# Optimization experiments

Hardware: AMD Instinct MI355X
Metric: run time of the kernel (lower is better)

## Reference

```python
import jax, jax.numpy as jnp
import numpy as np

PATCH = 9
EMBED = 768

def setup_inputs() -> dict:
    key = jax.random.key(0)
    k1, k2, k3, k4, k5, k6 = jax.random.split(key, 6)
    B, T, C, H, W = 4, 16, 3, 256, 256
    N = 8192
    patch_dim = PATCH * PATCH * C  # 243
    frames = jax.random.normal(k1, (B, T, C, H, W), dtype=jnp.float32)
    coords = jax.random.uniform(k2, (B, N, 2), dtype=jnp.float32)
    t_src = jax.random.randint(k3, (B, N), 0, T, dtype=jnp.int32)
    # MLP params (Linear: y = x @ W + b), kaiming-ish scale
    W1 = jax.random.normal(k4, (patch_dim, EMBED), dtype=jnp.float32) / np.sqrt(patch_dim)
    b1 = jnp.zeros((EMBED,), dtype=jnp.float32)
    W2 = jax.random.normal(k5, (EMBED, EMBED), dtype=jnp.float32) / np.sqrt(EMBED)
    b2 = jnp.zeros((EMBED,), dtype=jnp.float32)
    return {"frames": frames, "coords": coords, "t_src": t_src,
            "W1": W1, "b1": b1, "W2": W2, "b2": b2}

def reference(frames, coords, t_src, W1, b1, W2, b2):
    B, T, C, H, W = frames.shape
    N = coords.shape[1]
    half = PATCH // 2
    # integer center pixel (coords in [0,1] -> truncation == floor for nonneg)
    u = (coords[..., 0] * (W - 1)).astype(jnp.int32)  # (B, N)
    v = (coords[..., 1] * (H - 1)).astype(jnp.int32)
    off = jnp.arange(PATCH, dtype=jnp.int32) - half    # (P,)
    # replicate padding at borders == clamped gather indices
    ys = jnp.clip(v[..., None] + off, 0, H - 1)        # (B, N, P)
    xs = jnp.clip(u[..., None] + off, 0, W - 1)        # (B, N, P)
    fp = jnp.transpose(frames, (0, 1, 3, 4, 2))        # (B, T, H, W, C)
    bidx = jnp.arange(B, dtype=jnp.int32)[:, None, None, None]
    # gather patches: (B, N, P, P, C)
    patches = fp[bidx, t_src[:, :, None, None].astype(jnp.int32),
                 ys[:, :, :, None], xs[:, :, None, :]]
    x = patches.reshape(B, N, PATCH * PATCH * C)       # (B, N, 243)
    h = jax.nn.gelu(x @ W1 + b1, approximate=False)    # torch nn.GELU = exact erf
    return h @ W2 + b2                                 # (B, N, EMBED)
```

## Files before the change

### kernel.cpp

```cpp
#include <hip/hip_runtime.h>
#include <math.h>


typedef __attribute__((ext_vector_type(8))) short short8;
typedef __attribute__((ext_vector_type(4))) float floatx4;

#define M_ROWS 32768
#define KPAD   256
#define EMB    768

typedef __attribute__((address_space(1))) const void g_void;
typedef __attribute__((address_space(3))) void l_void;

__device__ __forceinline__ unsigned short f2bf(float f) {
    union { float f; unsigned int i; } w;
    w.f = f;
    unsigned int x = w.i;
    x += 0x7fffu + ((x >> 16) & 1u);
    return (unsigned short)(x >> 16);
}

__device__ __forceinline__ float gelu_f(float x) {
    float x3 = x * x * x;
    float y  = 1.5957691216f * (x + 0.044715f * x3);
    float e  = __expf(y);
    float th = 1.0f - 2.0f / (e + 1.0f);
    return 0.5f * x * (1.0f + th);
}

__global__ void k_transpose_w1(const float* __restrict__ W1,
                               unsigned short* __restrict__ W1T) {
    int idx = blockIdx.x * 256 + threadIdx.x;
    int n  = idx >> 8;
    int kp = idx & 255;
    unsigned short v = 0;
    if (kp < 243) {
        int c = kp / 81;
        int r = kp - c * 81;
        int i = r / 9;
        int j = r - i * 9;
        int e = i * 27 + j * 3 + c;
        v = f2bf(W1[e * EMB + n]);
    }
    W1T[idx] = v;
}

__global__ void k_transpose_w2(const float* __restrict__ W2,
                               unsigned short* __restrict__ W2T) {
    __shared__ float tile[32][33];
    int tx = threadIdx.x & 31, ty = threadIdx.x >> 5;
    int k0 = blockIdx.x * 32, n0 = blockIdx.y * 32;
#pragma unroll
    for (int i = 0; i < 4; ++i)
        tile[ty + i * 8][tx] = W2[(size_t)(k0 + ty + i * 8) * EMB + n0 + tx];
    __syncthreads();
#pragma unroll
    for (int i = 0; i < 4; ++i)
        W2T[(size_t)(n0 + ty + i * 8) * EMB + k0 + tx] = f2bf(tile[tx][ty + i * 8]);
}

__global__ void k_gather(const float* __restrict__ frames,
                         const float* __restrict__ coords,
                         const int* __restrict__ t_src,
                         unsigned short* __restrict__ X) {
    int row  = blockIdx.x * 4 + (threadIdx.x >> 6);
    int lane = threadIdx.x & 63;
    int b = row >> 13;

    float cu = coords[row * 2 + 0];
    float cv = coords[row * 2 + 1];
    int u = (int)(cu * 255.0f);
    int v = (int)(cv * 255.0f);
    int t = t_src[row];

    const float* fb = frames + (size_t)(b * 16 + t) * (3 * 256 * 256);
    unsigned short* xr = X + (size_t)row * KPAD;

#pragma unroll
    for (int it = 0; it < 4; ++it) {
        int kp = lane + it * 64;
        unsigned short val = 0;
        if (kp < 243) {
            int c = kp / 81;
            int r = kp - c * 81;
            int i = r / 9;
            int j = r - i * 9;
            int y = v + i - 4; y = (y < 0) ? 0 : (y > 255 ? 255 : y);
            int x = u + j - 4; x = (x < 0) ? 0 : (x > 255 ? 255 : x);
            val = f2bf(fb[(size_t)c * 65536 + y * 256 + x]);
        }
        xr[kp] = val;
    }
}

template <int K, bool GELU_, bool OUT_F32>
static __device__ __forceinline__
void gemm_body(const unsigned short* __restrict__ A,
               const unsigned short* __restrict__ BT,
               const float* __restrict__ bias,
               void* __restrict__ Cv) {
    __shared__ unsigned short As[2][128 * 64];
    __shared__ unsigned short Bs[2][128 * 64];

    const int tid  = threadIdx.x;
    const int wave = tid >> 6;
    const int lane = tid & 63;
    const int wr = wave >> 2;
    const int wc = wave & 3;
    const int lm = lane & 15;
    const int lq = lane >> 4;

    const int bid = blockIdx.x;
    const int swz = (bid & 7) * 192 + (bid >> 3);
    const int by  = swz % 6;
    const int bx  = swz / 6;
    const int m0 = bx * 128;
    const int n0 = by * 128;

    floatx4 acc[4][2];
#pragma unroll
    for (int i = 0; i < 4; ++i)
#pragma unroll
        for (int j = 0; j < 2; ++j)
            acc[i][j] = (floatx4){0.f, 0.f, 0.f, 0.f};

    const unsigned short* Ag = A  + (size_t)m0 * K;
    const unsigned short* Bg = BT + (size_t)n0 * K;

    const int rl    = lane >> 3;
    const int pl    = lane & 7;
    const int lslot = pl ^ rl;
    const int c0 = wave;
    const int c1 = 8 + wave;
    const size_t o0 = (size_t)(c0 * 8 + rl) * K + (lslot << 3);
    const size_t o1 = (size_t)(c1 * 8 + rl) * K + (lslot << 3);

    __builtin_amdgcn_global_load_lds((g_void*)(Ag + o0), (l_void*)(&As[0][c0 * 512]), 16, 0, 0);
    __builtin_amdgcn_global_load_lds((g_void*)(Ag + o1), (l_void*)(&As[0][c1 * 512]), 16, 0, 0);
    __builtin_amdgcn_global_load_lds((g_void*)(Bg + o0), (l_void*)(&Bs[0][c0 * 512]), 16, 0, 0);
    __builtin_amdgcn_global_load_lds((g_void*)(Bg + o1), (l_void*)(&Bs[0][c1 * 512]), 16, 0, 0);

    int buf = 0;
    for (int k0 = 0; k0 < K; k0 += 64) {
        __syncthreads();

        if (k0 + 64 < K) {
            __builtin_amdgcn_global_load_lds((g_void*)(Ag + o0 + k0 + 64),
                                             (l_void*)(&As[buf ^ 1][c0 * 512]), 16, 0, 0);
            __builtin_amdgcn_global_load_lds((g_void*)(Ag + o1 + k0 + 64),
                                             (l_void*)(&As[buf ^ 1][c1 * 512]), 16, 0, 0);
            __builtin_amdgcn_global_load_lds((g_void*)(Bg + o0 + k0 + 64),
                                             (l_void*)(&Bs[buf ^ 1][c0 * 512]), 16, 0, 0);
            __builtin_amdgcn_global_load_lds((g_void*)(Bg + o1 + k0 + 64),
                                             (l_void*)(&Bs[buf ^ 1][c1 * 512]), 16, 0, 0);
        }

#pragma unroll
        for (int ks = 0; ks < 2; ++ks) {
            short8 af[4], bfr[2];
#pragma unroll
            for (int mi = 0; mi < 4; ++mi) {
                int row = wr * 64 + mi * 16 + lm;
                int ps  = ((ks << 2) + lq) ^ (row & 7);
                af[mi] = *(const short8*)(&As[buf][row * 64 + (ps << 3)]);
            }
#pragma unroll
            for (int ni = 0; ni < 2; ++ni) {
                int row = wc * 32 + ni * 16 + lm;
                int ps  = ((ks << 2) + lq) ^ (row & 7);
                bfr[ni] = *(const short8*)(&Bs[buf][row * 64 + (ps << 3)]);
            }
#pragma unroll
            for (int mi = 0; mi < 4; ++mi)
#pragma unroll
                for (int ni = 0; ni < 2; ++ni)
                    acc[mi][ni] = __builtin_amdgcn_mfma_f32_16x16x32_bf16(
                        af[mi], bfr[ni], acc[mi][ni], 0, 0, 0);
        }
        buf ^= 1;
    }

#pragma unroll
    for (int ni = 0; ni < 2; ++ni) {
        int col = n0 + wc * 32 + ni * 16 + lm;
        float bs = bias[col];
#pragma unroll
        for (int mi = 0; mi < 4; ++mi) {
            int rowb = m0 + wr * 64 + mi * 16 + lq * 4;
#pragma unroll
            for (int r = 0; r < 4; ++r) {
                float x = acc[mi][ni][r] + bs;
                if (GELU_)
                    x = gelu_f(x);
                size_t idx = (size_t)(rowb + r) * EMB + col;
                if (OUT_F32)
                    ((float*)Cv)[idx] = x;
                else
                    ((unsigned short*)Cv)[idx] = f2bf(x);
            }
        }
    }
}

__global__ __launch_bounds__(512, 4)
void k_gemm1(const unsigned short* __restrict__ A, const unsigned short* __restrict__ BT,
             const float* __restrict__ bias, unsigned short* __restrict__ C) {
    gemm_body<KPAD, true, false>(A, BT, bias, (void*)C);
}

__global__ __launch_bounds__(512, 4)
void k_gemm2(const unsigned short* __restrict__ A, const unsigned short* __restrict__ BT,
             const float* __restrict__ bias, float* __restrict__ C) {
    gemm_body<EMB, false, true>(A, BT, bias, (void*)C);
}

extern "C" void kernel_launch(void* const* d_in, const int* in_sizes, int n_in,
                              void* d_out, int out_size, void* d_ws, size_t ws_size,
                              hipStream_t stream) {
    const float* frames = (const float*)d_in[0];
    const float* coords = (const float*)d_in[1];
    const int*   t_src  = (const int*)d_in[2];
    const float* W1     = (const float*)d_in[3];
    const float* b1     = (const float*)d_in[4];
    const float* W2     = (const float*)d_in[5];
    const float* b2     = (const float*)d_in[6];
    float* out = (float*)d_out;

    char* ws = (char*)d_ws;
    unsigned short* X    = (unsigned short*)(ws);
    unsigned short* Hbuf = (unsigned short*)(ws + 16777216);
    unsigned short* W1T  = (unsigned short*)(ws + 16777216 + 50331648);
    unsigned short* W2T  = (unsigned short*)(ws + 16777216 + 50331648 + 393216);

    k_transpose_w1<<<768, 256, 0, stream>>>(W1, W1T);
    k_transpose_w2<<<dim3(24, 24), 256, 0, stream>>>(W2, W2T);

    k_gather<<<M_ROWS / 4, 256, 0, stream>>>(frames, coords, t_src, X);

    k_gemm1<<<1536, 512, 0, stream>>>(X, W1T, b1, Hbuf);

    k_gemm2<<<1536, 512, 0, stream>>>(Hbuf, W2T, b2, out);
}
```

Baseline: 228.7 us.

## Restructure GEMM to 4 waves with 64x64 warp tiles and K-step 32

Reworks the GEMM kernels from 8 waves with 64x32 per-wave tiles and K-step 64 to 4 waves with 64x64 per-wave tiles and K-step 32. LDS gets a new swizzled layout and the fragment offsets are precomputed, which halves LDS use and raises register reuse per fragment load. Output stores switch to nontemporal writes to avoid polluting cache. The trade-off is more loop iterations and barriers per K, plus fewer threads per block to hide latency.

Result: slower. 286.8 us (+25.4%).

```diff
diff --git a/kernel.cpp b/kernel.cpp
--- a/kernel.cpp
+++ b/kernel.cpp
@@ -1,6 +1,8 @@
 #include <hip/hip_runtime.h>
 #include <math.h>
 
+
+#define USE_NT 1
 
 typedef __attribute__((ext_vector_type(8))) short short8;
 typedef __attribute__((ext_vector_type(4))) float floatx4;
@@ -99,14 +101,14 @@
                const unsigned short* __restrict__ BT,
                const float* __restrict__ bias,
                void* __restrict__ Cv) {
-    __shared__ unsigned short As[2][128 * 64];
-    __shared__ unsigned short Bs[2][128 * 64];
+    __shared__ unsigned short As[2][128 * 32];
+    __shared__ unsigned short Bs[2][128 * 32];
 
     const int tid  = threadIdx.x;
     const int wave = tid >> 6;
     const int lane = tid & 63;
-    const int wr = wave >> 2;
-    const int wc = wave & 3;
+    const int wm = (wave >> 1) * 64;
+    const int wn = (wave & 1) * 64;
     const int lm = lane & 15;
     const int lq = lane >> 4;
 
@@ -117,23 +119,30 @@
     const int m0 = bx * 128;
     const int n0 = by * 128;
 
-    floatx4 acc[4][2];
+    floatx4 acc[4][4];
 #pragma unroll
     for (int i = 0; i < 4; ++i)
 #pragma unroll
-        for (int j = 0; j < 2; ++j)
+        for (int j = 0; j < 4; ++j)
             acc[i][j] = (floatx4){0.f, 0.f, 0.f, 0.f};
 
     const unsigned short* Ag = A  + (size_t)m0 * K;
     const unsigned short* Bg = BT + (size_t)n0 * K;
 
-    const int rl    = lane >> 3;
-    const int pl    = lane & 7;
-    const int lslot = pl ^ rl;
-    const int c0 = wave;
-    const int c1 = 8 + wave;
-    const size_t o0 = (size_t)(c0 * 8 + rl) * K + (lslot << 3);
-    const size_t o1 = (size_t)(c1 * 8 + rl) * K + (lslot << 3);
+    const int rloc   = 2 * (lane >> 3) + ((lane >> 2) & 1);
+    const int kchunk = (lane & 3) ^ ((lane >> 3) & 3);
+    const int c0 = 2 * wave, c1 = 2 * wave + 1;
+    const size_t o0 = (size_t)(c0 * 16 + rloc) * K + (kchunk << 3);
+    const size_t o1 = (size_t)(c1 * 16 + rloc) * K + (kchunk << 3);
+
+    int aoff[4], boff[4];
+#pragma unroll
+    for (int mi = 0; mi < 4; ++mi) {
+        int r = wm + mi * 16 + lm;
+        aoff[mi] = (r >> 1) * 64 + (r & 1) * 32 + ((lq ^ ((r >> 1) & 3)) << 3);
+        int rb = wn + mi * 16 + lm;
+        boff[mi] = (rb >> 1) * 64 + (rb & 1) * 32 + ((lq ^ ((rb >> 1) & 3)) << 3);
+    }
 
     __builtin_amdgcn_global_load_lds((g_void*)(Ag + o0), (l_void*)(&As[0][c0 * 512]), 16, 0, 0);
     __builtin_amdgcn_global_load_lds((g_void*)(Ag + o1), (l_void*)(&As[0][c1 * 512]), 16, 0, 0);
@@ -141,74 +150,76 @@
     __builtin_amdgcn_global_load_lds((g_void*)(Bg + o1), (l_void*)(&Bs[0][c1 * 512]), 16, 0, 0);
 
     int buf = 0;
-    for (int k0 = 0; k0 < K; k0 += 64) {
+#pragma unroll 2
+    for (int k0 = 0; k0 < K; k0 += 32) {
         __syncthreads();
 
-        if (k0 + 64 < K) {
-            __builtin_amdgcn_global_load_lds((g_void*)(Ag + o0 + k0 + 64),
+        if (k0 + 32 < K) {
+            __builtin_amdgcn_global_load_lds((g_void*)(Ag + o0 + k0 + 32),
                                              (l_void*)(&As[buf ^ 1][c0 * 512]), 16, 0, 0);
-            __builtin_amdgcn_global_load_lds((g_void*)(Ag + o1 + k0 + 64),
+            __builtin_amdgcn_global_load_lds((g_void*)(Ag + o1 + k0 + 32),
                                              (l_void*)(&As[buf ^ 1][c1 * 512]), 16, 0, 0);
-            __builtin_amdgcn_global_load_lds((g_void*)(Bg + o0 + k0 + 64),
+            __builtin_amdgcn_global_load_lds((g_void*)(Bg + o0 + k0 + 32),
                                              (l_void*)(&Bs[buf ^ 1][c0 * 512]), 16, 0, 0);
-            __builtin_amdgcn_global_load_lds((g_void*)(Bg + o1 + k0 + 64),
+            __builtin_amdgcn_global_load_lds((g_void*)(Bg + o1 + k0 + 32),
                                              (l_void*)(&Bs[buf ^ 1][c1 * 512]), 16, 0, 0);
         }
 
-#pragma unroll
-        for (int ks = 0; ks < 2; ++ks) {
-            short8 af[4], bfr[2];
-#pragma unroll
-            for (int mi = 0; mi < 4; ++mi) {
-                int row = wr * 64 + mi * 16 + lm;
-                int ps  = ((ks << 2) + lq) ^ (row & 7);
-                af[mi] = *(const short8*)(&As[buf][row * 64 + (ps << 3)]);
-            }
-#pragma unroll
-            for (int ni = 0; ni < 2; ++ni) {
-                int row = wc * 32 + ni * 16 + lm;
-                int ps  = ((ks << 2) + lq) ^ (row & 7);
-                bfr[ni] = *(const short8*)(&Bs[buf][row * 64 + (ps << 3)]);
-            }
-#pragma unroll
-            for (int mi = 0; mi < 4; ++mi)
-#pragma unroll
-                for (int ni = 0; ni < 2; ++ni)
-                    acc[mi][ni] = __builtin_amdgcn_mfma_f32_16x16x32_bf16(
-                        af[mi], bfr[ni], acc[mi][ni], 0, 0, 0);
-        }
+        short8 af[4], bfr[4];
+#pragma unroll
+        for (int mi = 0; mi < 4; ++mi)
+            af[mi] = *(const short8*)(&As[buf][aoff[mi]]);
+#pragma unroll
+        for (int ni = 0; ni < 4; ++ni)
+            bfr[ni] = *(const short8*)(&Bs[buf][boff[ni]]);
+
+#pragma unroll
+        for (int mi = 0; mi < 4; ++mi)
+#pragma unroll
+            for (int ni = 0; ni < 4; ++ni)
+                acc[mi][ni] = __builtin_amdgcn_mfma_f32_16x16x32_bf16(
+                    af[mi], bfr[ni], acc[mi][ni], 0, 0, 0);
         buf ^= 1;
     }
 
 #pragma unroll
-    for (int ni = 0; ni < 2; ++ni) {
-        int col = n0 + wc * 32 + ni * 16 + lm;
+    for (int ni = 0; ni < 4; ++ni) {
+        int col = n0 + wn + ni * 16 + lm;
         float bs = bias[col];
 #pragma unroll
         for (int mi = 0; mi < 4; ++mi) {
-            int rowb = m0 + wr * 64 + mi * 16 + lq * 4;
+            int rowb = m0 + wm + mi * 16 + lq * 4;
 #pragma unroll
             for (int r = 0; r < 4; ++r) {
                 float x = acc[mi][ni][r] + bs;
                 if (GELU_)
                     x = gelu_f(x);
                 size_t idx = (size_t)(rowb + r) * EMB + col;
-                if (OUT_F32)
+                if (OUT_F32) {
+#if USE_NT
+                    __builtin_nontemporal_store(x, &((float*)Cv)[idx]);
+#else
                     ((float*)Cv)[idx] = x;
-                else
+#endif
+                } else {
+#if USE_NT
+                    __builtin_nontemporal_store(f2bf(x), &((unsigned short*)Cv)[idx]);
+#else
                     ((unsigned short*)Cv)[idx] = f2bf(x);
+#endif
+                }
             }
         }
     }
 }
 
-__global__ __launch_bounds__(512, 4)
+__global__ __launch_bounds__(256, 4)
 void k_gemm1(const unsigned short* __restrict__ A, const unsigned short* __restrict__ BT,
              const float* __restrict__ bias, unsigned short* __restrict__ C) {
     gemm_body<KPAD, true, false>(A, BT, bias, (void*)C);
 }
 
-__global__ __launch_bounds__(512, 4)
+__global__ __launch_bounds__(256, 4)
 void k_gemm2(const unsigned short* __restrict__ A, const unsigned short* __restrict__ BT,
              const float* __restrict__ bias, float* __restrict__ C) {
     gemm_body<EMB, false, true>(A, BT, bias, (void*)C);
@@ -237,7 +248,7 @@
 
     k_gather<<<M_ROWS / 4, 256, 0, stream>>>(frames, coords, t_src, X);
 
-    k_gemm1<<<1536, 512, 0, stream>>>(X, W1T, b1, Hbuf);
-
-    k_gemm2<<<1536, 512, 0, stream>>>(Hbuf, W2T, b2, out);
-}
+    k_gemm1<<<1536, 256, 0, stream>>>(X, W1T, b1, Hbuf);
+
+    k_gemm2<<<1536, 256, 0, stream>>>(Hbuf, W2T, b2, out);
+}
```

## Widen GEMM tiles to 128x256 with single-buffered LDS and early fragment loads

Applied to the files above, without the earlier changes.

Doubles the N dimension of each GEMM block tile from 128 to 256, giving each wave a 64x64 output sub-tile with 16 accumulators, and halves the grid to 768 blocks. LDS drops from double buffers to a single buffer. The second k-half fragments are read into registers before a barrier so the next stage's global-to-LDS loads can overlap the second half of the MFMA work. LDS offsets are precomputed. The larger tile raises reuse per load but increases register pressure, leaves fewer blocks for the CUs, and exposes more load latency through the single buffer and extra barriers.

Result: no change. 230.5 us (+0.8%).

```diff
diff --git a/kernel.cpp b/kernel.cpp
--- a/kernel.cpp
+++ b/kernel.cpp
@@ -99,8 +99,8 @@
                const unsigned short* __restrict__ BT,
                const float* __restrict__ bias,
                void* __restrict__ Cv) {
-    __shared__ unsigned short As[2][128 * 64];
-    __shared__ unsigned short Bs[2][128 * 64];
+    __shared__ unsigned short As[128 * 64];
+    __shared__ unsigned short Bs[256 * 64];
 
     const int tid  = threadIdx.x;
     const int wave = tid >> 6;
@@ -111,17 +111,17 @@
     const int lq = lane >> 4;
 
     const int bid = blockIdx.x;
-    const int swz = (bid & 7) * 192 + (bid >> 3);
-    const int by  = swz % 6;
-    const int bx  = swz / 6;
+    const int swz = (bid & 7) * 96 + (bid >> 3);
+    const int by  = swz % 3;
+    const int bx  = swz / 3;
     const int m0 = bx * 128;
-    const int n0 = by * 128;
-
-    floatx4 acc[4][2];
+    const int n0 = by * 256;
+
+    floatx4 acc[4][4];
 #pragma unroll
     for (int i = 0; i < 4; ++i)
 #pragma unroll
-        for (int j = 0; j < 2; ++j)
+        for (int j = 0; j < 4; ++j)
             acc[i][j] = (floatx4){0.f, 0.f, 0.f, 0.f};
 
     const unsigned short* Ag = A  + (size_t)m0 * K;
@@ -130,59 +130,81 @@
     const int rl    = lane >> 3;
     const int pl    = lane & 7;
     const int lslot = pl ^ rl;
-    const int c0 = wave;
-    const int c1 = 8 + wave;
-    const size_t o0 = (size_t)(c0 * 8 + rl) * K + (lslot << 3);
-    const size_t o1 = (size_t)(c1 * 8 + rl) * K + (lslot << 3);
-
-    __builtin_amdgcn_global_load_lds((g_void*)(Ag + o0), (l_void*)(&As[0][c0 * 512]), 16, 0, 0);
-    __builtin_amdgcn_global_load_lds((g_void*)(Ag + o1), (l_void*)(&As[0][c1 * 512]), 16, 0, 0);
-    __builtin_amdgcn_global_load_lds((g_void*)(Bg + o0), (l_void*)(&Bs[0][c0 * 512]), 16, 0, 0);
-    __builtin_amdgcn_global_load_lds((g_void*)(Bg + o1), (l_void*)(&Bs[0][c1 * 512]), 16, 0, 0);
-
-    int buf = 0;
+    const size_t so = (size_t)(lslot << 3);
+    const size_t oA0 = (size_t)((wave)      * 8 + rl) * K + so;
+    const size_t oA1 = (size_t)((wave + 8)  * 8 + rl) * K + so;
+    const size_t oB0 = (size_t)((wave)      * 8 + rl) * K + so;
+    const size_t oB1 = (size_t)((wave + 8)  * 8 + rl) * K + so;
+    const size_t oB2 = (size_t)((wave + 16) * 8 + rl) * K + so;
+    const size_t oB3 = (size_t)((wave + 24) * 8 + rl) * K + so;
+
+    int aoff[2][4], boff[2][4];
+#pragma unroll
+    for (int mi = 0; mi < 4; ++mi) {
+        int ra = wr * 64 + mi * 16 + lm;
+        int rb = wc * 64 + mi * 16 + lm;
+#pragma unroll
+        for (int ks = 0; ks < 2; ++ks) {
+            aoff[ks][mi] = ra * 64 + ((((ks << 2) + lq) ^ (ra & 7)) << 3);
+            boff[ks][mi] = rb * 64 + ((((ks << 2) + lq) ^ (rb & 7)) << 3);
+        }
+    }
+
+#define STAGE(K0) do {                                                         \
+    __builtin_amdgcn_global_load_lds((g_void*)(Ag + oA0 + (K0)),               \
+        (l_void*)(&As[(wave)      * 512]), 16, 0, 0);                          \
+    __builtin_amdgcn_global_load_lds((g_void*)(Ag + oA1 + (K0)),               \
+        (l_void*)(&As[(wave + 8)  * 512]), 16, 0, 0);                          \
+    __builtin_amdgcn_global_load_lds((g_void*)(Bg + oB0 + (K0)),               \
+        (l_void*)(&Bs[(wave)      * 512]), 16, 0, 0);                          \
+    __builtin_amdgcn_global_load_lds((g_void*)(Bg + oB1 + (K0)),               \
+        (l_void*)(&Bs[(wave + 8)  * 512]), 16, 0, 0);                          \
+    __builtin_amdgcn_global_load_lds((g_void*)(Bg + oB2 + (K0)),               \
+        (l_void*)(&Bs[(wave + 16) * 512]), 16, 0, 0);                          \
+    __builtin_amdgcn_global_load_lds((g_void*)(Bg + oB3 + (K0)),               \
+        (l_void*)(&Bs[(wave + 24) * 512]), 16, 0, 0);                          \
+} while (0)
+
+    STAGE(0);
+    __syncthreads();
+
+#pragma unroll 1
     for (int k0 = 0; k0 < K; k0 += 64) {
+        short8 fa0[4], fb0[4], fa1[4], fb1[4];
+#pragma unroll
+        for (int mi = 0; mi < 4; ++mi) fa0[mi] = *(const short8*)(&As[aoff[0][mi]]);
+#pragma unroll
+        for (int ni = 0; ni < 4; ++ni) fb0[ni] = *(const short8*)(&Bs[boff[0][ni]]);
+#pragma unroll
+        for (int mi = 0; mi < 4; ++mi)
+#pragma unroll
+            for (int ni = 0; ni < 4; ++ni)
+                acc[mi][ni] = __builtin_amdgcn_mfma_f32_16x16x32_bf16(
+                    fa0[mi], fb0[ni], acc[mi][ni], 0, 0, 0);
+#pragma unroll
+        for (int mi = 0; mi < 4; ++mi) fa1[mi] = *(const short8*)(&As[aoff[1][mi]]);
+#pragma unroll
+        for (int ni = 0; ni < 4; ++ni) fb1[ni] = *(const short8*)(&Bs[boff[1][ni]]);
+
         __syncthreads();
-
-        if (k0 + 64 < K) {
-            __builtin_amdgcn_global_load_lds((g_void*)(Ag + o0 + k0 + 64),
-                                             (l_void*)(&As[buf ^ 1][c0 * 512]), 16, 0, 0);
-            __builtin_amdgcn_global_load_lds((g_void*)(Ag + o1 + k0 + 64),
-                                             (l_void*)(&As[buf ^ 1][c1 * 512]), 16, 0, 0);
-            __builtin_amdgcn_global_load_lds((g_void*)(Bg + o0 + k0 + 64),
-                                             (l_void*)(&Bs[buf ^ 1][c0 * 512]), 16, 0, 0);
-            __builtin_amdgcn_global_load_lds((g_void*)(Bg + o1 + k0 + 64),
-                                             (l_void*)(&Bs[buf ^ 1][c1 * 512]), 16, 0, 0);
-        }
-
-#pragma unroll
-        for (int ks = 0; ks < 2; ++ks) {
-            short8 af[4], bfr[2];
-#pragma unroll
-            for (int mi = 0; mi < 4; ++mi) {
-                int row = wr * 64 + mi * 16 + lm;
-                int ps  = ((ks << 2) + lq) ^ (row & 7);
-                af[mi] = *(const short8*)(&As[buf][row * 64 + (ps << 3)]);
-            }
-#pragma unroll
-            for (int ni = 0; ni < 2; ++ni) {
-                int row = wc * 32 + ni * 16 + lm;
-                int ps  = ((ks << 2) + lq) ^ (row & 7);
-                bfr[ni] = *(const short8*)(&Bs[buf][row * 64 + (ps << 3)]);
-            }
-#pragma unroll
-            for (int mi = 0; mi < 4; ++mi)
-#pragma unroll
-                for (int ni = 0; ni < 2; ++ni)
-                    acc[mi][ni] = __builtin_amdgcn_mfma_f32_16x16x32_bf16(
-                        af[mi], bfr[ni], acc[mi][ni], 0, 0, 0);
-        }
-        buf ^= 1;
-    }
-
-#pragma unroll
-    for (int ni = 0; ni < 2; ++ni) {
-        int col = n0 + wc * 32 + ni * 16 + lm;
+        if (k0 + 64 < K)
+            STAGE(k0 + 64);
+
+#pragma unroll
+        for (int mi = 0; mi < 4; ++mi)
+#pragma unroll
+            for (int ni = 0; ni < 4; ++ni)
+                acc[mi][ni] = __builtin_amdgcn_mfma_f32_16x16x32_bf16(
+                    fa1[mi], fb1[ni], acc[mi][ni], 0, 0, 0);
+
+        if (k0 + 64 < K)
+            __syncthreads();
+    }
+#undef STAGE
+
+#pragma unroll
+    for (int ni = 0; ni < 4; ++ni) {
+        int col = n0 + wc * 64 + ni * 16 + lm;
         float bs = bias[col];
 #pragma unroll
         for (int mi = 0; mi < 4; ++mi) {
@@ -237,7 +259,7 @@
 
     k_gather<<<M_ROWS / 4, 256, 0, stream>>>(frames, coords, t_src, X);
 
-    k_gemm1<<<1536, 512, 0, stream>>>(X, W1T, b1, Hbuf);
-
-    k_gemm2<<<1536, 512, 0, stream>>>(Hbuf, W2T, b2, out);
-}
+    k_gemm1<<<768, 512, 0, stream>>>(X, W1T, b1, Hbuf);
+
+    k_gemm2<<<768, 512, 0, stream>>>(Hbuf, W2T, b2, out);
+}
```
